# Performance work log

Measured on AMD Instinct MI355X. Metric: run time of the kernel, lower is better.

Reference implementation:

```python
import jax, jax.numpy as jnp
import numpy as np

B = 16384
N_NEIGH = 50
D = 64
NUM_USERS = 100000
NUM_ITEMS = 100000
NUM_ENTITIES = 200000


def setup_inputs() -> dict:
    key = jax.random.key(0)
    ks = jax.random.split(key, 16)
    s = 1.0 / np.sqrt(D)
    return {
        "user_indices": jax.random.randint(ks[0], (B,), 0, NUM_USERS),
        "item_indices": jax.random.randint(ks[1], (B,), 0, NUM_ITEMS),
        "kg_adj_batch": jax.random.randint(ks[2], (B, N_NEIGH), 0, NUM_ENTITIES),
        "user_table": jax.random.normal(ks[3], (NUM_USERS, D), jnp.float32),
        "item_table": jax.random.normal(ks[4], (NUM_ITEMS, D), jnp.float32),
        "entity_table": jax.random.normal(ks[5], (NUM_ENTITIES, D), jnp.float32),
        "attn_W": jax.random.normal(ks[6], (2 * D, 1), jnp.float32) * s,
        "attn_b": jnp.zeros((1,), jnp.float32),
        "kg_W1": jax.random.normal(ks[7], (D, D), jnp.float32) * s,
        "kg_b1": jnp.zeros((D,), jnp.float32),
        "kg_W2": jax.random.normal(ks[8], (D, D), jnp.float32) * s,
        "kg_b2": jnp.zeros((D,), jnp.float32),
        "comb_W": jax.random.normal(ks[9], (2 * D, D), jnp.float32) * s,
        "comb_b": jnp.zeros((D,), jnp.float32),
        "out_W": jax.random.normal(ks[10], (2 * D, 1), jnp.float32) * s,
        "out_b": jnp.zeros((1,), jnp.float32),
    }


def reference(user_indices, item_indices, kg_adj_batch,
              user_table, item_table, entity_table,
              attn_W, attn_b, kg_W1, kg_b1, kg_W2, kg_b2,
              comb_W, comb_b, out_W, out_b):
    user_emb = user_table[user_indices]          # [B, D]
    item_emb = item_table[item_indices]          # [B, D]
    nbr_idx = jnp.clip(kg_adj_batch, 0)
    neighbor_emb = entity_table[nbr_idx]         # [B, N, D]
    # attention_linear(cat([item, nbr])) == item @ Wi + nbr @ Wn + b (avoids [B,N,2D])
    Wi, Wn = attn_W[:D], attn_W[D:]
    attn_scores = item_emb @ Wi + jnp.einsum('bnd,do->bno', neighbor_emb, Wn)[..., 0] + attn_b  # [B, N]
    attn_scores = jax.nn.leaky_relu(attn_scores, negative_slope=0.2)
    attn_weights = jax.nn.softmax(attn_scores, axis=1)                 # softmax over neighbors
    neighbor_attn = jnp.einsum('bn,bnd->bd', attn_weights, neighbor_emb)
    refined_kg = jax.nn.relu(neighbor_attn @ kg_W1 + kg_b1) @ kg_W2 + kg_b2
    combined_item = jnp.concatenate([item_emb, refined_kg], axis=1)
    final_item_rep = jax.nn.relu(combined_item @ comb_W + comb_b)      # dropout = identity (eval)
    combined_user_item = jnp.concatenate([user_emb, final_item_rep], axis=1)
    score = (combined_user_item @ out_W + out_b)[:, 0]
    return score
```

## Files before the change

### kernel.cpp

```cpp
#include <hip/hip_runtime.h>

#define NN 50
#define D 64
#define GRP 10

typedef unsigned int uint32;
typedef unsigned short ushort16;

__device__ __forceinline__ float wave_sum64(float x) {
#pragma unroll
  for (int off = 32; off > 0; off >>= 1)
    x += __shfl_xor(x, off, 64);
  return x;
}

__device__ __forceinline__ float readlane_f(float v, int l) {
  return __uint_as_float(__builtin_amdgcn_readlane(__float_as_uint(v), l));
}

__device__ __forceinline__ ushort16 f32_to_bf16(float f) {
  uint32 u = __float_as_uint(f);
  u += 0x7FFF + ((u >> 16) & 1);
  return (ushort16)(u >> 16);
}
__device__ __forceinline__ float bf16_to_f32(ushort16 h) {
  return __uint_as_float(((uint32)h) << 16);
}

__global__ __launch_bounds__(256, 4) void ent_proj(
    const float* __restrict__ ent_tab, const float* __restrict__ attn_W,
    float* __restrict__ proj, ushort16* __restrict__ ent_bf, int rows)
{
  const int  lane = threadIdx.x & 63;
  const long wave = (long)blockIdx.x * 4 + (threadIdx.x >> 6);
  const long base = wave * GRP;
  if (base >= rows) return;
  const float Wn = attn_W[D + lane];
  float v[GRP];
#pragma unroll
  for (int i = 0; i < GRP; ++i) {
    long r = base + i; if (r > rows - 1) r = rows - 1;
    v[i] = ent_tab[r * D + lane];
  }
  float s[GRP];
#pragma unroll
  for (int i = 0; i < GRP; ++i)
    s[i] = wave_sum64(v[i] * Wn);
#pragma unroll
  for (int i = 0; i < GRP; ++i) {
    const long r = base + i;
    if (r < rows) ent_bf[r * D + lane] = f32_to_bf16(v[i]);
  }
  if (lane == 0) {
#pragma unroll
    for (int i = 0; i < GRP; ++i)
      if (base + i < rows) proj[base + i] = s[i];
  }
}

__device__ __forceinline__ void load_grp_bf(float (&buf)[GRP],
                                            const int* __restrict__ adjb,
                                            const ushort16* __restrict__ ent_bf,
                                            int g, int lane) {
#pragma unroll
  for (int i = 0; i < GRP; ++i) {
    int t = adjb[g * GRP + i];
    t = t < 0 ? 0 : t;
    buf[i] = bf16_to_f32(ent_bf[(long)t * D + lane]);
  }
}

__device__ __forceinline__ void acc_grp(const float (&buf)[GRP], float e, int g,
                                        float& na0, float& na1) {
#pragma unroll
  for (int i = 0; i < GRP; ++i) {
    const float w = readlane_f(e, g * GRP + i);
    if (i & 1) na1 = fmaf(w, buf[i], na1);
    else       na0 = fmaf(w, buf[i], na0);
  }
}

__global__ __launch_bounds__(256, 4) void kgat_attn(
    const int* __restrict__ item_idx, const int* __restrict__ adj,
    const float* __restrict__ item_tab,
    const ushort16* __restrict__ ent_bf, const float* __restrict__ proj,
    const float* __restrict__ attn_W, const float* __restrict__ attn_b,
    float* __restrict__ naws, int B)
{
  const int lane = threadIdx.x & 63;
  const int wv   = threadIdx.x >> 6;
  const int b    = blockIdx.x * 4 + wv;
  if (b >= B) return;

  const int* adjb = adj + (long)b * NN;

  float A[GRP], Bv[GRP];
  load_grp_bf(A,  adjb, ent_bf, 0, lane);
  load_grp_bf(Bv, adjb, ent_bf, 1, lane);

  const float item = item_tab[(long)item_idx[b] * D + lane];
  const float base = wave_sum64(item * attn_W[lane]) + attn_b[0];

  const int myn = lane < NN ? lane : NN - 1;
  int mi = adjb[myn]; mi = mi < 0 ? 0 : mi;
  float s = proj[mi] + base;
  s = s > 0.f ? s : 0.2f * s;
  const float e = (lane < NN) ? __expf(s - 8.0f) : 0.f;
  const float denom = wave_sum64(e);

  float na0 = 0.f, na1 = 0.f;
  acc_grp(A,  e, 0, na0, na1);
  load_grp_bf(A,  adjb, ent_bf, 2, lane);
  acc_grp(Bv, e, 1, na0, na1);
  load_grp_bf(Bv, adjb, ent_bf, 3, lane);
  acc_grp(A,  e, 2, na0, na1);
  load_grp_bf(A,  adjb, ent_bf, 4, lane);
  acc_grp(Bv, e, 3, na0, na1);
  acc_grp(A,  e, 4, na0, na1);

  naws[(long)b * D + lane] = (na0 + na1) / denom;
}

__global__ __launch_bounds__(256, 4) void kgat_mlp2(
    const int* __restrict__ user_idx, const int* __restrict__ item_idx,
    const float* __restrict__ user_tab, const float* __restrict__ item_tab,
    const float* __restrict__ naws,
    const float* __restrict__ W1, const float* __restrict__ b1,
    const float* __restrict__ W2, const float* __restrict__ b2,
    const float* __restrict__ cW, const float* __restrict__ cb,
    const float* __restrict__ oW, const float* __restrict__ ob,
    float* __restrict__ out, int B)
{
  __shared__ __align__(16) float s_a0[4 * D], s_a1[4 * D];
  __shared__ __align__(16) float s_i0[4 * D], s_i1[4 * D];

  const int lane = threadIdx.x & 63;
  const int wv   = threadIdx.x >> 6;
  const int bA   = (blockIdx.x * 4 + wv) * 2;
  if (bA >= B) return;
  const int bB   = bA + 1 < B ? bA + 1 : bA;
  float* sa0 = s_a0 + wv * D;
  float* sa1 = s_a1 + wv * D;
  float* si0 = s_i0 + wv * D;
  float* si1 = s_i1 + wv * D;

  const float naA = naws[(long)bA * D + lane];
  const float naB = naws[(long)bB * D + lane];
  const float itA = item_tab[(long)item_idx[bA] * D + lane];
  const float itB = item_tab[(long)item_idx[bB] * D + lane];
  const float usA = user_tab[(long)user_idx[bA] * D + lane];
  const float usB = user_tab[(long)user_idx[bB] * D + lane];

  sa0[lane] = naA; sa1[lane] = naB;
  si0[lane] = itA; si1[lane] = itB;

  const float b1v = b1[lane];
  float hA0 = b1v, hA1 = 0.f, hA2 = 0.f, hA3 = 0.f;
  float hB0 = b1v, hB1 = 0.f, hB2 = 0.f, hB3 = 0.f;
#pragma unroll
  for (int d = 0; d < D; d += 4) {
    const float4 cA = *(const float4*)(sa0 + d);
    const float4 cB = *(const float4*)(sa1 + d);
    const float w0 = W1[(d + 0) * D + lane];
    const float w1 = W1[(d + 1) * D + lane];
    const float w2 = W1[(d + 2) * D + lane];
    const float w3 = W1[(d + 3) * D + lane];
    hA0 = fmaf(cA.x, w0, hA0); hB0 = fmaf(cB.x, w0, hB0);
    hA1 = fmaf(cA.y, w1, hA1); hB1 = fmaf(cB.y, w1, hB1);
    hA2 = fmaf(cA.z, w2, hA2); hB2 = fmaf(cB.z, w2, hB2);
    hA3 = fmaf(cA.w, w3, hA3); hB3 = fmaf(cB.w, w3, hB3);
  }
  const float hA = fmaxf((hA0 + hA1) + (hA2 + hA3), 0.f);
  const float hB = fmaxf((hB0 + hB1) + (hB2 + hB3), 0.f);

  sa0[lane] = hA; sa1[lane] = hB;
  const float b2v = b2[lane];
  float rA0 = b2v, rA1 = 0.f, rA2 = 0.f, rA3 = 0.f;
  float rB0 = b2v, rB1 = 0.f, rB2 = 0.f, rB3 = 0.f;
#pragma unroll
  for (int d = 0; d < D; d += 4) {
    const float4 cA = *(const float4*)(sa0 + d);
    const float4 cB = *(const float4*)(sa1 + d);
    const float w0 = W2[(d + 0) * D + lane];
    const float w1 = W2[(d + 1) * D + lane];
    const float w2 = W2[(d + 2) * D + lane];
    const float w3 = W2[(d + 3) * D + lane];
    rA0 = fmaf(cA.x, w0, rA0); rB0 = fmaf(cB.x, w0, rB0);
    rA1 = fmaf(cA.y, w1, rA1); rB1 = fmaf(cB.y, w1, rB1);
    rA2 = fmaf(cA.z, w2, rA2); rB2 = fmaf(cB.z, w2, rB2);
    rA3 = fmaf(cA.w, w3, rA3); rB3 = fmaf(cB.w, w3, rB3);
  }
  const float rA = (rA0 + rA1) + (rA2 + rA3);
  const float rB = (rB0 + rB1) + (rB2 + rB3);

  sa0[lane] = rA; sa1[lane] = rB;
  const float cbv = cb[lane];
  float fA0 = cbv, fA1 = 0.f, fA2 = 0.f, fA3 = 0.f;
  float fB0 = cbv, fB1 = 0.f, fB2 = 0.f, fB3 = 0.f;
#pragma unroll
  for (int k = 0; k < D; k += 4) {
    const float4 cA = *(const float4*)(si0 + k);
    const float4 cB = *(const float4*)(si1 + k);
    const float w0 = cW[(k + 0) * D + lane];
    const float w1 = cW[(k + 1) * D + lane];
    const float w2 = cW[(k + 2) * D + lane];
    const float w3 = cW[(k + 3) * D + lane];
    fA0 = fmaf(cA.x, w0, fA0); fB0 = fmaf(cB.x, w0, fB0);
    fA1 = fmaf(cA.y, w1, fA1); fB1 = fmaf(cB.y, w1, fB1);
    fA2 = fmaf(cA.z, w2, fA2); fB2 = fmaf(cB.z, w2, fB2);
    fA3 = fmaf(cA.w, w3, fA3); fB3 = fmaf(cB.w, w3, fB3);
  }
#pragma unroll
  for (int k = 0; k < D; k += 4) {
    const float4 cA = *(const float4*)(sa0 + k);
    const float4 cB = *(const float4*)(sa1 + k);
    const float w0 = cW[(D + k + 0) * D + lane];
    const float w1 = cW[(D + k + 1) * D + lane];
    const float w2 = cW[(D + k + 2) * D + lane];
    const float w3 = cW[(D + k + 3) * D + lane];
    fA0 = fmaf(cA.x, w0, fA0); fB0 = fmaf(cB.x, w0, fB0);
    fA1 = fmaf(cA.y, w1, fA1); fB1 = fmaf(cB.y, w1, fB1);
    fA2 = fmaf(cA.z, w2, fA2); fB2 = fmaf(cB.z, w2, fB2);
    fA3 = fmaf(cA.w, w3, fA3); fB3 = fmaf(cB.w, w3, fB3);
  }
  const float fA = fmaxf((fA0 + fA1) + (fA2 + fA3), 0.f);
  const float fB = fmaxf((fB0 + fB1) + (fB2 + fB3), 0.f);

  const float oWu = oW[lane];
  const float oWf = oW[D + lane];
  const float ob0 = ob[0];
  const float scA = wave_sum64(fmaf(usA, oWu, fA * oWf));
  const float scB = wave_sum64(fmaf(usB, oWu, fB * oWf));
  if (lane == 0) {
    out[bA] = scA + ob0;
    if (bB != bA) out[bB] = scB + ob0;
  }
}

__device__ __forceinline__ void load_grp(float (&buf)[GRP],
                                         const int* __restrict__ adjb,
                                         const float* __restrict__ ent_tab,
                                         int g, int lane) {
#pragma unroll
  for (int i = 0; i < GRP; ++i) {
    int t = adjb[g * GRP + i];
    t = t < 0 ? 0 : t;
    buf[i] = ent_tab[(long)t * D + lane];
  }
}

__device__ __forceinline__ void proc_grp(const float (&buf)[GRP],
                                         float Wn, float base,
                                         float& l0, float& l1, float& na) {
  float ex[GRP];
#pragma unroll
  for (int i = 0; i < GRP; ++i) {
    float t = wave_sum64(buf[i] * Wn) + base;
    t = t > 0.f ? t : 0.2f * t;
    ex[i] = __expf(t - 8.0f);
  }
#pragma unroll
  for (int i = 0; i < GRP; ++i) {
    if (i & 1) l1 += ex[i]; else l0 += ex[i];
    na = fmaf(ex[i], buf[i], na);
  }
}

__global__ __launch_bounds__(256, 4) void kgat_r3(
    const int* __restrict__ user_idx, const int* __restrict__ item_idx,
    const int* __restrict__ adj,
    const float* __restrict__ user_tab, const float* __restrict__ item_tab,
    const float* __restrict__ ent_tab,
    const float* __restrict__ attn_W, const float* __restrict__ attn_b,
    const float* __restrict__ W1, const float* __restrict__ b1,
    const float* __restrict__ W2, const float* __restrict__ b2,
    const float* __restrict__ cW, const float* __restrict__ cb,
    const float* __restrict__ oW, const float* __restrict__ ob,
    float* __restrict__ out, int B)
{
  const int lane = threadIdx.x & 63;
  const int wv   = threadIdx.x >> 6;
  const int b    = blockIdx.x * 4 + wv;
  if (b >= B) return;

  const float user = user_tab[(long)user_idx[b] * D + lane];
  const float oWu  = oW[lane];
  const float oWf  = oW[D + lane];
  const float item = item_tab[(long)item_idx[b] * D + lane];
  const float Wi   = attn_W[lane];
  const float Wn   = attn_W[D + lane];
  const float base = wave_sum64(item * Wi) + attn_b[0];
  const int* adjb = adj + b * NN;

  float na = 0.f, l0 = 0.f, l1 = 0.f;
  float A[GRP], Bv[GRP];
  load_grp(A,  adjb, ent_tab, 0, lane);
  load_grp(Bv, adjb, ent_tab, 1, lane);
  proc_grp(A,  Wn, base, l0, l1, na);
  load_grp(A,  adjb, ent_tab, 2, lane);
  proc_grp(Bv, Wn, base, l0, l1, na);
  load_grp(Bv, adjb, ent_tab, 3, lane);
  proc_grp(A,  Wn, base, l0, l1, na);
  load_grp(A,  adjb, ent_tab, 4, lane);
  proc_grp(Bv, Wn, base, l0, l1, na);
  proc_grp(A,  Wn, base, l0, l1, na);
  na /= (l0 + l1);

  float h0 = b1[lane], h1 = 0.f, h2 = 0.f, h3 = 0.f;
#pragma unroll
  for (int d = 0; d < D; d += 4) {
    h0 = fmaf(readlane_f(na, d + 0), W1[(d + 0) * D + lane], h0);
    h1 = fmaf(readlane_f(na, d + 1), W1[(d + 1) * D + lane], h1);
    h2 = fmaf(readlane_f(na, d + 2), W1[(d + 2) * D + lane], h2);
    h3 = fmaf(readlane_f(na, d + 3), W1[(d + 3) * D + lane], h3);
  }
  const float h = fmaxf((h0 + h1) + (h2 + h3), 0.f);

  float r0 = b2[lane], r1 = 0.f, r2 = 0.f, r3 = 0.f;
#pragma unroll
  for (int d = 0; d < D; d += 4) {
    r0 = fmaf(readlane_f(h, d + 0), W2[(d + 0) * D + lane], r0);
    r1 = fmaf(readlane_f(h, d + 1), W2[(d + 1) * D + lane], r1);
    r2 = fmaf(readlane_f(h, d + 2), W2[(d + 2) * D + lane], r2);
    r3 = fmaf(readlane_f(h, d + 3), W2[(d + 3) * D + lane], r3);
  }
  const float r = (r0 + r1) + (r2 + r3);

  float f0 = cb[lane], f1 = 0.f, f2 = 0.f, f3 = 0.f;
#pragma unroll
  for (int k = 0; k < D; k += 4) {
    f0 = fmaf(readlane_f(item, k + 0), cW[(k + 0) * D + lane], f0);
    f1 = fmaf(readlane_f(item, k + 1), cW[(k + 1) * D + lane], f1);
    f2 = fmaf(readlane_f(item, k + 2), cW[(k + 2) * D + lane], f2);
    f3 = fmaf(readlane_f(item, k + 3), cW[(k + 3) * D + lane], f3);
  }
#pragma unroll
  for (int k = 0; k < D; k += 4) {
    f0 = fmaf(readlane_f(r, k + 0), cW[(D + k + 0) * D + lane], f0);
    f1 = fmaf(readlane_f(r, k + 1), cW[(D + k + 1) * D + lane], f1);
    f2 = fmaf(readlane_f(r, k + 2), cW[(D + k + 2) * D + lane], f2);
    f3 = fmaf(readlane_f(r, k + 3), cW[(D + k + 3) * D + lane], f3);
  }
  const float f = fmaxf((f0 + f1) + (f2 + f3), 0.f);

  const float sc = wave_sum64(fmaf(user, oWu, f * oWf));
  if (lane == 0) out[b] = sc + ob[0];
}

extern "C" void kernel_launch(void* const* d_in, const int* in_sizes, int n_in,
                              void* d_out, int out_size, void* d_ws, size_t ws_size,
                              hipStream_t stream) {
  const int*   user_idx = (const int*)d_in[0];
  const int*   item_idx = (const int*)d_in[1];
  const int*   adj      = (const int*)d_in[2];
  const float* user_tab = (const float*)d_in[3];
  const float* item_tab = (const float*)d_in[4];
  const float* ent_tab  = (const float*)d_in[5];
  const float* attn_W   = (const float*)d_in[6];
  const float* attn_b   = (const float*)d_in[7];
  const float* W1       = (const float*)d_in[8];
  const float* b1       = (const float*)d_in[9];
  const float* W2       = (const float*)d_in[10];
  const float* b2       = (const float*)d_in[11];
  const float* cW       = (const float*)d_in[12];
  const float* cb       = (const float*)d_in[13];
  const float* oW       = (const float*)d_in[14];
  const float* ob       = (const float*)d_in[15];
  float* out = (float*)d_out;

  const int B    = in_sizes[0];
  const int rows = in_sizes[5] / D;

  const size_t off_bf = ((size_t)rows * 4 + 255) & ~(size_t)255;
  const size_t off_na = (off_bf + (size_t)rows * D * 2 + 255) & ~(size_t)255;
  const size_t need   = off_na + (size_t)B * D * 4;

  if (ws_size >= need) {
    float*    proj   = (float*)d_ws;
    ushort16* ent_bf = (ushort16*)((char*)d_ws + off_bf);
    float*    naws   = (float*)((char*)d_ws + off_na);
    const int waves   = (rows + GRP - 1) / GRP;
    const int pblocks = (waves + 3) / 4;
    const int ablocks = (B + 3) / 4;
    const int mblocks = (B + 7) / 8;
    ent_proj<<<pblocks, 256, 0, stream>>>(ent_tab, attn_W, proj, ent_bf, rows);
    kgat_attn<<<ablocks, 256, 0, stream>>>(item_idx, adj, item_tab, ent_bf,
                                           proj, attn_W, attn_b, naws, B);
    kgat_mlp2<<<mblocks, 256, 0, stream>>>(user_idx, item_idx, user_tab,
                                           item_tab, naws, W1, b1, W2, b2,
                                           cW, cb, oW, ob, out, B);
  } else {
    const int blocks = (B + 3) / 4;
    kgat_r3<<<blocks, 256, 0, stream>>>(user_idx, item_idx, adj,
                                        user_tab, item_tab, ent_tab,
                                        attn_W, attn_b, W1, b1, W2, b2,
                                        cW, cb, oW, ob, out, B);
  }
}
```

Baseline: 62.31 us.

## Process four rows per wave in MLP kernel using readlane broadcasts

The MLP stage now has each wave handle four batch rows instead of two. Every weight load is therefore reused across four rows, and the grid shrinks by half. Activation broadcasts now use v_readlane into scalar operands instead of writing to and reading back from shared memory. This drops LDS traffic and the shared-memory round-trips, but adds register pressure and scalar readlane instructions.

```diff
diff --git a/kernel.cpp b/kernel.cpp
--- a/kernel.cpp
+++ b/kernel.cpp
@@ -121,7 +121,7 @@
   naws[(long)b * D + lane] = (na0 + na1) / denom;
 }
 
-__global__ __launch_bounds__(256, 4) void kgat_mlp2(
+__global__ __launch_bounds__(256, 4) void kgat_mlp4r(
     const int* __restrict__ user_idx, const int* __restrict__ item_idx,
     const float* __restrict__ user_tab, const float* __restrict__ item_tab,
     const float* __restrict__ naws,
@@ -131,109 +131,117 @@
     const float* __restrict__ oW, const float* __restrict__ ob,
     float* __restrict__ out, int B)
 {
-  __shared__ __align__(16) float s_a0[4 * D], s_a1[4 * D];
-  __shared__ __align__(16) float s_i0[4 * D], s_i1[4 * D];
-
   const int lane = threadIdx.x & 63;
   const int wv   = threadIdx.x >> 6;
-  const int bA   = (blockIdx.x * 4 + wv) * 2;
-  if (bA >= B) return;
-  const int bB   = bA + 1 < B ? bA + 1 : bA;
-  float* sa0 = s_a0 + wv * D;
-  float* sa1 = s_a1 + wv * D;
-  float* si0 = s_i0 + wv * D;
-  float* si1 = s_i1 + wv * D;
+  const int b0   = (blockIdx.x * 4 + wv) * 4;
+  if (b0 >= B) return;
+
+  const int bA = b0 + 0 < B ? b0 + 0 : B - 1;
+  const int bB = b0 + 1 < B ? b0 + 1 : B - 1;
+  const int bC = b0 + 2 < B ? b0 + 2 : B - 1;
+  const int bD = b0 + 3 < B ? b0 + 3 : B - 1;
 
   const float naA = naws[(long)bA * D + lane];
   const float naB = naws[(long)bB * D + lane];
+  const float naC = naws[(long)bC * D + lane];
+  const float naD = naws[(long)bD * D + lane];
   const float itA = item_tab[(long)item_idx[bA] * D + lane];
   const float itB = item_tab[(long)item_idx[bB] * D + lane];
+  const float itC = item_tab[(long)item_idx[bC] * D + lane];
+  const float itD = item_tab[(long)item_idx[bD] * D + lane];
   const float usA = user_tab[(long)user_idx[bA] * D + lane];
   const float usB = user_tab[(long)user_idx[bB] * D + lane];
-
-  sa0[lane] = naA; sa1[lane] = naB;
-  si0[lane] = itA; si1[lane] = itB;
+  const float usC = user_tab[(long)user_idx[bC] * D + lane];
+  const float usD = user_tab[(long)user_idx[bD] * D + lane];
 
   const float b1v = b1[lane];
-  float hA0 = b1v, hA1 = 0.f, hA2 = 0.f, hA3 = 0.f;
-  float hB0 = b1v, hB1 = 0.f, hB2 = 0.f, hB3 = 0.f;
-#pragma unroll
-  for (int d = 0; d < D; d += 4) {
-    const float4 cA = *(const float4*)(sa0 + d);
-    const float4 cB = *(const float4*)(sa1 + d);
-    const float w0 = W1[(d + 0) * D + lane];
-    const float w1 = W1[(d + 1) * D + lane];
-    const float w2 = W1[(d + 2) * D + lane];
-    const float w3 = W1[(d + 3) * D + lane];
-    hA0 = fmaf(cA.x, w0, hA0); hB0 = fmaf(cB.x, w0, hB0);
-    hA1 = fmaf(cA.y, w1, hA1); hB1 = fmaf(cB.y, w1, hB1);
-    hA2 = fmaf(cA.z, w2, hA2); hB2 = fmaf(cB.z, w2, hB2);
-    hA3 = fmaf(cA.w, w3, hA3); hB3 = fmaf(cB.w, w3, hB3);
-  }
-  const float hA = fmaxf((hA0 + hA1) + (hA2 + hA3), 0.f);
-  const float hB = fmaxf((hB0 + hB1) + (hB2 + hB3), 0.f);
-
-  sa0[lane] = hA; sa1[lane] = hB;
+  float hA0 = b1v, hA1 = 0.f, hB0 = b1v, hB1 = 0.f;
+  float hC0 = b1v, hC1 = 0.f, hD0 = b1v, hD1 = 0.f;
+#pragma unroll
+  for (int k = 0; k < D; k += 2) {
+    const float w0 = W1[(k + 0) * D + lane];
+    const float w1 = W1[(k + 1) * D + lane];
+    hA0 = fmaf(readlane_f(naA, k + 0), w0, hA0);
+    hA1 = fmaf(readlane_f(naA, k + 1), w1, hA1);
+    hB0 = fmaf(readlane_f(naB, k + 0), w0, hB0);
+    hB1 = fmaf(readlane_f(naB, k + 1), w1, hB1);
+    hC0 = fmaf(readlane_f(naC, k + 0), w0, hC0);
+    hC1 = fmaf(readlane_f(naC, k + 1), w1, hC1);
+    hD0 = fmaf(readlane_f(naD, k + 0), w0, hD0);
+    hD1 = fmaf(readlane_f(naD, k + 1), w1, hD1);
+  }
+  const float hA = fmaxf(hA0 + hA1, 0.f);
+  const float hB = fmaxf(hB0 + hB1, 0.f);
+  const float hC = fmaxf(hC0 + hC1, 0.f);
+  const float hD = fmaxf(hD0 + hD1, 0.f);
+
   const float b2v = b2[lane];
-  float rA0 = b2v, rA1 = 0.f, rA2 = 0.f, rA3 = 0.f;
-  float rB0 = b2v, rB1 = 0.f, rB2 = 0.f, rB3 = 0.f;
-#pragma unroll
-  for (int d = 0; d < D; d += 4) {
-    const float4 cA = *(const float4*)(sa0 + d);
-    const float4 cB = *(const float4*)(sa1 + d);
-    const float w0 = W2[(d + 0) * D + lane];
-    const float w1 = W2[(d + 1) * D + lane];
-    const float w2 = W2[(d + 2) * D + lane];
-    const float w3 = W2[(d + 3) * D + lane];
-    rA0 = fmaf(cA.x, w0, rA0); rB0 = fmaf(cB.x, w0, rB0);
-    rA1 = fmaf(cA.y, w1, rA1); rB1 = fmaf(cB.y, w1, rB1);
-    rA2 = fmaf(cA.z, w2, rA2); rB2 = fmaf(cB.z, w2, rB2);
-    rA3 = fmaf(cA.w, w3, rA3); rB3 = fmaf(cB.w, w3, rB3);
-  }
-  const float rA = (rA0 + rA1) + (rA2 + rA3);
-  const float rB = (rB0 + rB1) + (rB2 + rB3);
-
-  sa0[lane] = rA; sa1[lane] = rB;
+  float rA0 = b2v, rA1 = 0.f, rB0 = b2v, rB1 = 0.f;
+  float rC0 = b2v, rC1 = 0.f, rD0 = b2v, rD1 = 0.f;
+#pragma unroll
+  for (int k = 0; k < D; k += 2) {
+    const float w0 = W2[(k + 0) * D + lane];
+    const float w1 = W2[(k + 1) * D + lane];
+    rA0 = fmaf(readlane_f(hA, k + 0), w0, rA0);
+    rA1 = fmaf(readlane_f(hA, k + 1), w1, rA1);
+    rB0 = fmaf(readlane_f(hB, k + 0), w0, rB0);
+    rB1 = fmaf(readlane_f(hB, k + 1), w1, rB1);
+    rC0 = fmaf(readlane_f(hC, k + 0), w0, rC0);
+    rC1 = fmaf(readlane_f(hC, k + 1), w1, rC1);
+    rD0 = fmaf(readlane_f(hD, k + 0), w0, rD0);
+    rD1 = fmaf(readlane_f(hD, k + 1), w1, rD1);
+  }
+  const float rA = rA0 + rA1;
+  const float rB = rB0 + rB1;
+  const float rC = rC0 + rC1;
+  const float rD = rD0 + rD1;
+
   const float cbv = cb[lane];
-  float fA0 = cbv, fA1 = 0.f, fA2 = 0.f, fA3 = 0.f;
-  float fB0 = cbv, fB1 = 0.f, fB2 = 0.f, fB3 = 0.f;
-#pragma unroll
-  for (int k = 0; k < D; k += 4) {
-    const float4 cA = *(const float4*)(si0 + k);
-    const float4 cB = *(const float4*)(si1 + k);
+  float fA0 = cbv, fA1 = 0.f, fB0 = cbv, fB1 = 0.f;
+  float fC0 = cbv, fC1 = 0.f, fD0 = cbv, fD1 = 0.f;
+#pragma unroll
+  for (int k = 0; k < D; k += 2) {
     const float w0 = cW[(k + 0) * D + lane];
     const float w1 = cW[(k + 1) * D + lane];
-    const float w2 = cW[(k + 2) * D + lane];
-    const float w3 = cW[(k + 3) * D + lane];
-    fA0 = fmaf(cA.x, w0, fA0); fB0 = fmaf(cB.x, w0, fB0);
-    fA1 = fmaf(cA.y, w1, fA1); fB1 = fmaf(cB.y, w1, fB1);
-    fA2 = fmaf(cA.z, w2, fA2); fB2 = fmaf(cB.z, w2, fB2);
-    fA3 = fmaf(cA.w, w3, fA3); fB3 = fmaf(cB.w, w3, fB3);
-  }
-#pragma unroll
-  for (int k = 0; k < D; k += 4) {
-    const float4 cA = *(const float4*)(sa0 + k);
-    const float4 cB = *(const float4*)(sa1 + k);
+    fA0 = fmaf(readlane_f(itA, k + 0), w0, fA0);
+    fA1 = fmaf(readlane_f(itA, k + 1), w1, fA1);
+    fB0 = fmaf(readlane_f(itB, k + 0), w0, fB0);
+    fB1 = fmaf(readlane_f(itB, k + 1), w1, fB1);
+    fC0 = fmaf(readlane_f(itC, k + 0), w0, fC0);
+    fC1 = fmaf(readlane_f(itC, k + 1), w1, fC1);
+    fD0 = fmaf(readlane_f(itD, k + 0), w0, fD0);
+    fD1 = fmaf(readlane_f(itD, k + 1), w1, fD1);
+  }
+#pragma unroll
+  for (int k = 0; k < D; k += 2) {
     const float w0 = cW[(D + k + 0) * D + lane];
     const float w1 = cW[(D + k + 1) * D + lane];
-    const float w2 = cW[(D + k + 2) * D + lane];
-    const float w3 = cW[(D + k + 3) * D + lane];
-    fA0 = fmaf(cA.x, w0, fA0); fB0 = fmaf(cB.x, w0, fB0);
-    fA1 = fmaf(cA.y, w1, fA1); fB1 = fmaf(cB.y, w1, fB1);
-    fA2 = fmaf(cA.z, w2, fA2); fB2 = fmaf(cB.z, w2, fB2);
-    fA3 = fmaf(cA.w, w3, fA3); fB3 = fmaf(cB.w, w3, fB3);
-  }
-  const float fA = fmaxf((fA0 + fA1) + (fA2 + fA3), 0.f);
-  const float fB = fmaxf((fB0 + fB1) + (fB2 + fB3), 0.f);
+    fA0 = fmaf(readlane_f(rA, k + 0), w0, fA0);
+    fA1 = fmaf(readlane_f(rA, k + 1), w1, fA1);
+    fB0 = fmaf(readlane_f(rB, k + 0), w0, fB0);
+    fB1 = fmaf(readlane_f(rB, k + 1), w1, fB1);
+    fC0 = fmaf(readlane_f(rC, k + 0), w0, fC0);
+    fC1 = fmaf(readlane_f(rC, k + 1), w1, fC1);
+    fD0 = fmaf(readlane_f(rD, k + 0), w0, fD0);
+    fD1 = fmaf(readlane_f(rD, k + 1), w1, fD1);
+  }
+  const float fA = fmaxf(fA0 + fA1, 0.f);
+  const float fB = fmaxf(fB0 + fB1, 0.f);
+  const float fC = fmaxf(fC0 + fC1, 0.f);
+  const float fD = fmaxf(fD0 + fD1, 0.f);
 
   const float oWu = oW[lane];
   const float oWf = oW[D + lane];
   const float ob0 = ob[0];
   const float scA = wave_sum64(fmaf(usA, oWu, fA * oWf));
   const float scB = wave_sum64(fmaf(usB, oWu, fB * oWf));
+  const float scC = wave_sum64(fmaf(usC, oWu, fC * oWf));
+  const float scD = wave_sum64(fmaf(usD, oWu, fD * oWf));
   if (lane == 0) {
     out[bA] = scA + ob0;
     if (bB != bA) out[bB] = scB + ob0;
+    if (bC != bB) out[bC] = scC + ob0;
+    if (bD != bC) out[bD] = scD + ob0;
   }
 }
 
@@ -382,13 +390,13 @@
     const int waves   = (rows + GRP - 1) / GRP;
     const int pblocks = (waves + 3) / 4;
     const int ablocks = (B + 3) / 4;
-    const int mblocks = (B + 7) / 8;
+    const int mblocks = (B + 15) / 16;
     ent_proj<<<pblocks, 256, 0, stream>>>(ent_tab, attn_W, proj, ent_bf, rows);
     kgat_attn<<<ablocks, 256, 0, stream>>>(item_idx, adj, item_tab, ent_bf,
                                            proj, attn_W, attn_b, naws, B);
-    kgat_mlp2<<<mblocks, 256, 0, stream>>>(user_idx, item_idx, user_tab,
-                                           item_tab, naws, W1, b1, W2, b2,
-                                           cW, cb, oW, ob, out, B);
+    kgat_mlp4r<<<mblocks, 256, 0, stream>>>(user_idx, item_idx, user_tab,
+                                            item_tab, naws, W1, b1, W2, b2,
+                                            cW, cb, oW, ob, out, B);
   } else {
     const int blocks = (B + 3) / 4;
     kgat_r3<<<blocks, 256, 0, stream>>>(user_idx, item_idx, adj,
```

After: 66.74 us. 1.07x slower.
